# Kernel tuning notes

Hardware: AMD Instinct MI355X
Metric: run time of the kernel (lower is better)

## Reference

```python
import jax, jax.numpy as jnp
import numpy as np

B, C, H, W = 16, 512, 32, 32
NH, HD = 8, 64
CTX_DIM, L = 768, 512
EPS = 1e-5


def setup_inputs() -> dict:
    key = jax.random.key(0)
    ks = jax.random.split(key, 10)
    x = jax.random.normal(ks[0], (B, C, H, W), dtype=jnp.float32)
    context = jax.random.normal(ks[1], (B, L, CTX_DIM), dtype=jnp.float32)
    context_mask = jax.random.randint(ks[2], (B, L), 0, 2).astype(bool)
    context_mask = context_mask.at[:, 0].set(True)  # guarantee >=1 valid key per row
    s = 0.02
    ln_w = jnp.ones((C,), jnp.float32)
    ln_b = jnp.zeros((C,), jnp.float32)
    Wq = jax.random.normal(ks[3], (C, C), jnp.float32) * s
    Wk = jax.random.normal(ks[4], (C, C), jnp.float32) * s
    Wv = jax.random.normal(ks[5], (C, C), jnp.float32) * s
    Wo = jax.random.normal(ks[6], (C, C), jnp.float32) * s
    Wctx = jax.random.normal(ks[7], (C, CTX_DIM), jnp.float32) * s
    return {"x": x, "context": context, "context_mask": context_mask,
            "ln_w": ln_w, "ln_b": ln_b, "Wq": Wq, "Wk": Wk, "Wv": Wv,
            "Wo": Wo, "Wctx": Wctx}


def _layernorm(x, w, b):
    mu = jnp.mean(x, axis=-1, keepdims=True)
    var = jnp.mean(jnp.square(x - mu), axis=-1, keepdims=True)
    return (x - mu) * jax.lax.rsqrt(var + EPS) * w + b


def reference(x, context, context_mask, ln_w, ln_b, Wq, Wk, Wv, Wo, Wctx):
    b, c, h, w = x.shape
    n = h * w
    hidden = x.reshape(b, c, n).transpose(0, 2, 1)          # [b, n, c]
    hidden_norm = _layernorm(hidden, ln_w, ln_b)
    ctx = jnp.einsum('bld,cd->blc', context, Wctx)          # context_proj

    q = jnp.einsum('bnc,ec->bne', hidden_norm, Wq).reshape(b, n, NH, HD).transpose(0, 2, 1, 3)
    k = jnp.einsum('blc,ec->ble', ctx, Wk).reshape(b, -1, NH, HD).transpose(0, 2, 1, 3)
    v = jnp.einsum('blc,ec->ble', ctx, Wv).reshape(b, -1, NH, HD).transpose(0, 2, 1, 3)

    scale = HD ** -0.5
    scores = jnp.einsum('bhnd,bhld->bhnl', q, k) * scale    # [b,H,n,L]
    mask4 = context_mask[:, None, None, :]                  # [b,1,1,L]
    scores = jnp.where(mask4, scores, -jnp.inf)
    all_invalid = ~jnp.any(mask4, axis=-1, keepdims=True)   # [b,1,1,1]
    scores = jnp.where(all_invalid, 0.0, scores)
    attn = jax.nn.softmax(scores, axis=-1)
    attn = jnp.where(mask4, attn, 0.0)
    attn = jnp.where(all_invalid, 0.0, attn)

    out = jnp.einsum('bhnl,bhld->bhnd', attn, v)            # [b,H,n,hd]
    out = out.transpose(0, 2, 1, 3).reshape(b, n, c)
    out = jnp.einsum('bnc,ec->bne', out, Wo)
    out = out + hidden
    return out.transpose(0, 2, 1).reshape(b, c, h, w)
```

## Files before the change

### kernel.cpp

```cpp
#include <hip/hip_runtime.h>

#define B_   16
#define C_   512
#define N_   1024
#define L_   512
#define CTX_ 768
#define NH_  8
#define HD_  64
#define EPS_ 1e-5f

typedef short bfrag  __attribute__((ext_vector_type(8)));
typedef short bfrag4 __attribute__((ext_vector_type(4)));
typedef float f32x4  __attribute__((ext_vector_type(4)));

__device__ __forceinline__ ushort f2bf(float f) {
  union { float f; unsigned u; } v; v.f = f;
  unsigned r = v.u + 0x7fffu + ((v.u >> 16) & 1u);
  return (ushort)(r >> 16);
}

__device__ __forceinline__ f32x4 mfma16(bfrag a, bfrag b, f32x4 c) {
  return __builtin_amdgcn_mfma_f32_16x16x32_bf16(a, b, c, 0, 0, 0);
}
__device__ __forceinline__ f32x4 mfma16k16(bfrag4 a, bfrag4 b, f32x4 c) {
  return __builtin_amdgcn_mfma_f32_16x16x16bf16_1k(a, b, c, 0, 0, 0);
}
__device__ __forceinline__ unsigned cvt_pk_bf16(float lo, float hi) {
  unsigned d;
  asm("v_cvt_pk_bf16_f32 %0, %1, %2" : "=v"(d) : "v"(lo), "v"(hi));
  return d;
}

__device__ __forceinline__ void g2l16(const ushort* g, ushort* l) {
  __builtin_amdgcn_global_load_lds(
      (const __attribute__((address_space(1))) void*)g,
      (__attribute__((address_space(3))) void*)l, 16, 0, 0);
}

__global__ __launch_bounds__(256) void cast6_kernel(
    const float* __restrict__ s0, const float* __restrict__ s1,
    const float* __restrict__ s2, const float* __restrict__ s3,
    const float* __restrict__ s4, const float* __restrict__ s5,
    ushort* __restrict__ d0, ushort* __restrict__ d1, ushort* __restrict__ d2,
    ushort* __restrict__ d3, ushort* __restrict__ d4, ushort* __restrict__ d5) {
  int i = blockIdx.x * 256 + threadIdx.x;
  const float* src; ushort* dst; int off;
  if      (i < 1572864) { src = s0; dst = d0; off = i; }
  else if (i < 1671168) { src = s1; dst = d1; off = i - 1572864; }
  else if (i < 1736704) { src = s2; dst = d2; off = i - 1671168; }
  else if (i < 1802240) { src = s3; dst = d3; off = i - 1736704; }
  else if (i < 1867776) { src = s4; dst = d4; off = i - 1802240; }
  else                  { src = s5; dst = d5; off = i - 1867776; }
  float4 vv = ((const float4*)src)[off];
  ushort4 o;
  o.x = f2bf(vv.x); o.y = f2bf(vv.y); o.z = f2bf(vv.z); o.w = f2bf(vv.w);
  ((ushort4*)dst)[off] = o;
}

__global__ __launch_bounds__(1024) void ln_kernel(const float* __restrict__ x,
                                                  const float* __restrict__ w,
                                                  const float* __restrict__ bia,
                                                  ushort* __restrict__ hn) {
  const int b  = blockIdx.x;
  const int n0 = blockIdx.y * 64;
  const int tid = threadIdx.x;
  const int nx = tid & 63, cg = tid >> 6;
  const float* xb = x + (size_t)b * C_ * N_;

  float s = 0.f, s2 = 0.f;
  for (int c = cg; c < C_; c += 16) {
    float v = xb[(size_t)c * N_ + n0 + nx];
    s += v; s2 += v * v;
  }
  __shared__ float red[2][16][64];
  __shared__ float mean[64], rstd[64];
  red[0][cg][nx] = s; red[1][cg][nx] = s2;
  __syncthreads();
  if (cg == 0) {
    float ss = 0.f, ss2 = 0.f;
#pragma unroll
    for (int i = 0; i < 16; ++i) { ss += red[0][i][nx]; ss2 += red[1][i][nx]; }
    float mu  = ss * (1.f / C_);
    float var = ss2 * (1.f / C_) - mu * mu;
    mean[nx] = mu;
    rstd[nx] = rsqrtf(var + EPS_);
  }
  __syncthreads();

  __shared__ float tile[64][65];
  for (int ct = 0; ct < 8; ++ct) {
    const int c0 = ct * 64;
    for (int cy = cg; cy < 64; cy += 16)
      tile[cy][nx] = xb[(size_t)(c0 + cy) * N_ + n0 + nx];
    __syncthreads();
    const int cx = tid & 63, ng = tid >> 6;
    const float wv = w[c0 + cx], bv = bia[c0 + cx];
    for (int ny = ng; ny < 64; ny += 16) {
      float val = (tile[cx][ny] - mean[ny]) * rstd[ny] * wv + bv;
      hn[((size_t)b * N_ + n0 + ny) * C_ + c0 + cx] = f2bf(val);
    }
    __syncthreads();
  }
}

__device__ __forceinline__ void gemm_core(const ushort* __restrict__ A,
                                          const ushort* __restrict__ W,
                                          int K, ushort* la, ushort* lb,
                                          f32x4 acc[4][4],
                                          int tid, int wm, int we, int col, int rg) {
  const int lane = tid & 63, w = tid >> 6;
  const int rloc = lane >> 2, pt = lane & 3;
  const int pts = pt ^ ((rloc >> 1) & 3);
  const int qsel = (rg ^ ((col >> 1) & 3)) * 8;

  for (int k0 = 0; k0 < K; k0 += 32) {
#pragma unroll
    for (int c = 0; c < 2; ++c) {
      const int chunk = w + c * 4;
      const int row = chunk * 16 + rloc;
      g2l16(A + (size_t)row * K + k0 + pts * 8, la + chunk * 512);
      g2l16(W + (size_t)row * K + k0 + pts * 8, lb + chunk * 512);
    }
    __syncthreads();
    bfrag af[4], bf[4];
#pragma unroll
    for (int i = 0; i < 4; ++i) {
      af[i] = *(const bfrag*)&la[(wm + i * 16 + col) * 32 + qsel];
      bf[i] = *(const bfrag*)&lb[(we + i * 16 + col) * 32 + qsel];
    }
#pragma unroll
    for (int i = 0; i < 4; ++i)
#pragma unroll
      for (int j = 0; j < 4; ++j)
        acc[i][j] = mfma16(af[i], bf[j], acc[i][j]);
    __syncthreads();
  }
}

__global__ __launch_bounds__(256) void gemm_ctxq(const ushort* __restrict__ ctxb,
                                                 const ushort* __restrict__ Wctxb,
                                                 ushort* __restrict__ ctxo,
                                                 const ushort* __restrict__ hn,
                                                 const ushort* __restrict__ Wqb,
                                                 ushort* __restrict__ qo) {
  __shared__ ushort la[128 * 32];
  __shared__ ushort lb[128 * 32];
  const int bid = blockIdx.x;
  const int tid = threadIdx.x, lane = tid & 63, w = tid >> 6;
  const int wm = (w >> 1) * 64, we = (w & 1) * 64;
  const int col = lane & 15, rg = lane >> 4;

  const ushort* A; const ushort* W; ushort* out; int K, m0, e0;
  if (bid < 256) {
    m0 = (bid & 63) * 128; e0 = (bid >> 6) * 128;
    A = ctxb; W = Wctxb; out = ctxo; K = CTX_;
  } else {
    const int b2 = bid - 256;
    m0 = (b2 & 127) * 128; e0 = (b2 >> 7) * 128;
    A = hn; W = Wqb; out = qo; K = C_;
  }

  f32x4 acc[4][4] = {};
  gemm_core(A + (size_t)m0 * K, W + (size_t)e0 * K, K, la, lb, acc, tid, wm, we, col, rg);

#pragma unroll
  for (int i = 0; i < 4; ++i)
#pragma unroll
    for (int j = 0; j < 4; ++j)
#pragma unroll
      for (int r = 0; r < 4; ++r)
        out[(size_t)(m0 + wm + i * 16 + rg * 4 + r) * 512 + e0 + we + j * 16 + col] =
            f2bf(acc[i][j][r]);
}

__global__ __launch_bounds__(256) void gemm_kv(const ushort* __restrict__ A,
                                               const ushort* __restrict__ Wk,
                                               const ushort* __restrict__ Wv,
                                               ushort* __restrict__ Ko,
                                               ushort* __restrict__ Vt_g) {
  __shared__ ushort la[128 * 32];
  __shared__ ushort lb[128 * 32];
  __shared__ float T[16][132];
  const int isv = blockIdx.y >> 2;
  const ushort* W = isv ? Wv : Wk;
  const int m0 = blockIdx.x * 128, e0 = (blockIdx.y & 3) * 128;
  const int tid = threadIdx.x, lane = tid & 63, w = tid >> 6;
  const int wm = (w >> 1) * 64, we = (w & 1) * 64;
  const int col = lane & 15, rg = lane >> 4;

  f32x4 acc[4][4] = {};
  gemm_core(A + (size_t)m0 * C_, W + (size_t)e0 * C_, C_, la, lb, acc, tid, wm, we, col, rg);

  if (!isv) {
#pragma unroll
    for (int i = 0; i < 4; ++i)
#pragma unroll
      for (int j = 0; j < 4; ++j)
#pragma unroll
        for (int r = 0; r < 4; ++r)
          Ko[(size_t)(m0 + wm + i * 16 + rg * 4 + r) * 512 + e0 + we + j * 16 + col] =
              f2bf(acc[i][j][r]);
  } else {
    const int b = m0 >> 9, l0 = m0 & 511;
#pragma unroll
    for (int g = 0; g < 8; ++g) {
      if ((w & 1) == (g >> 2)) {
        const int j = g & 3;
#pragma unroll
        for (int i = 0; i < 4; ++i)
          *(f32x4*)&T[col][wm + i * 16 + rg * 4] = acc[i][j];
      }
      __syncthreads();
      const int n = tid & 127;
      for (int cc = tid >> 7; cc < 16; cc += 2) {
        const int e = e0 + g * 16 + cc;
        Vt_g[((size_t)b * 512 + e) * 512 + l0 + n] = f2bf(T[cc][n]);
      }
      __syncthreads();
    }
  }
}

__global__ __launch_bounds__(256) void gemm_res(const ushort* __restrict__ A,
                                                const ushort* __restrict__ W,
                                                const float* __restrict__ x,
                                                float* __restrict__ out) {
  __shared__ ushort la[128 * 32];
  __shared__ ushort lb[128 * 32];
  __shared__ float T[16][132];
  const int m0 = blockIdx.x * 128, e0 = blockIdx.y * 128;
  const int tid = threadIdx.x, lane = tid & 63, w = tid >> 6;
  const int wm = (w >> 1) * 64, we = (w & 1) * 64;
  const int col = lane & 15, rg = lane >> 4;

  f32x4 acc[4][4] = {};
  gemm_core(A + (size_t)m0 * C_, W + (size_t)e0 * C_, C_, la, lb, acc, tid, wm, we, col, rg);

  const int b = m0 >> 10, n0l = m0 & 1023;
#pragma unroll
  for (int g = 0; g < 8; ++g) {
    if ((w & 1) == (g >> 2)) {
      const int j = g & 3;
#pragma unroll
      for (int i = 0; i < 4; ++i)
        *(f32x4*)&T[col][wm + i * 16 + rg * 4] = acc[i][j];
    }
    __syncthreads();
    const int n = tid & 127;
    for (int cc = tid >> 7; cc < 16; cc += 2) {
      const int c = e0 + g * 16 + cc;
      const size_t idx = (size_t)b * C_ * N_ + (size_t)c * N_ + n0l + n;
      out[idx] = T[cc][n] + x[idx];
    }
    __syncthreads();
  }
}

__global__ __launch_bounds__(256) void attn_mfma(const ushort* __restrict__ q,
                                                 const ushort* __restrict__ k,
                                                 const ushort* __restrict__ vt,
                                                 const int* __restrict__ mask,
                                                 ushort* __restrict__ o) {
  __shared__ ushort Kl[2][64 * 72];
  __shared__ ushort Vt[2][64 * 72];
  __shared__ float mlb[2][64];

  const int lin = blockIdx.x;
  const int hb = lin & 127, qb = lin >> 7;
  const int h = hb & 7, b = hb >> 3;
  const int q0 = qb * 128;
  const int tid = threadIdx.x, lane = tid & 63, w = tid >> 6;
  const int col = lane & 15, rg = lane >> 4;
  const int wq = w * 32;
  const float C1 = 0.18033688011112042f;

  bfrag qf[2][2];
#pragma unroll
  for (int mi = 0; mi < 2; ++mi)
#pragma unroll
    for (int kc = 0; kc < 2; ++kc)
      qf[mi][kc] = *(const bfrag*)
          &q[((size_t)b * N_ + q0 + wq + mi * 16 + col) * C_ + h * HD_ + kc * 32 + rg * 8];

  f32x4 oa[2][4] = {};
  float l_part[2] = {0.f, 0.f};

  {
#pragma unroll
    for (int it = 0; it < 2; ++it) {
      const int idx = it * 256 + tid;
      const int key = idx >> 3, part = idx & 7;
      *(int4*)&Kl[0][key * 72 + part * 8] =
          *(const int4*)&k[((size_t)b * L_ + key) * C_ + h * HD_ + part * 8];
    }
#pragma unroll
    for (int it = 0; it < 2; ++it) {
      const int idx = it * 256 + tid;
      const int d = idx >> 3, k8 = (idx & 7) * 8;
      *(int4*)&Vt[0][d * 72 + k8] =
          *(const int4*)&vt[((size_t)b * 512 + h * HD_ + d) * 512 + k8];
    }
    if (tid < 64) mlb[0][tid] = mask[b * L_ + tid] ? 0.f : -1e30f;
  }
  __syncthreads();

  for (int t = 0; t < 8; ++t) {
    const int cur = t & 1;
    int4 kreg[2];
    int4 vreg[2];
    float mreg = 0.f;
    if (t < 7) {
      const int l0n = (t + 1) * 64;
#pragma unroll
      for (int it = 0; it < 2; ++it) {
        const int idx = it * 256 + tid;
        const int key = idx >> 3, part = idx & 7;
        kreg[it] = *(const int4*)&k[((size_t)b * L_ + l0n + key) * C_ + h * HD_ + part * 8];
      }
#pragma unroll
      for (int it = 0; it < 2; ++it) {
        const int idx = it * 256 + tid;
        const int d = idx >> 3, k8 = (idx & 7) * 8;
        vreg[it] = *(const int4*)&vt[((size_t)b * 512 + h * HD_ + d) * 512 + l0n + k8];
      }
      if (tid < 64) mreg = mask[b * L_ + l0n + tid] ? 0.f : -1e30f;
    }

    const ushort* Kc = &Kl[cur][0];
    const ushort* Vc = &Vt[cur][0];
    f32x4 s2[2][4] = {};
#pragma unroll
    for (int kc = 0; kc < 2; ++kc) {
      bfrag kf[4];
#pragma unroll
      for (int ni = 0; ni < 4; ++ni)
        kf[ni] = *(const bfrag*)&Kc[(ni * 16 + col) * 72 + kc * 32 + rg * 8];
#pragma unroll
      for (int mi = 0; mi < 2; ++mi)
#pragma unroll
        for (int ni = 0; ni < 4; ++ni)
          s2[mi][ni] = mfma16(kf[ni], qf[mi][kc], s2[mi][ni]);
    }
    bfrag4 pf[2][4];
#pragma unroll
    for (int ni = 0; ni < 4; ++ni) {
      const f32x4 bias4 = *(const f32x4*)&mlb[cur][ni * 16 + rg * 4];
#pragma unroll
      for (int mi = 0; mi < 2; ++mi) {
        const float p0 = exp2f(fmaf(s2[mi][ni][0], C1, bias4[0]));
        const float p1 = exp2f(fmaf(s2[mi][ni][1], C1, bias4[1]));
        const float p2 = exp2f(fmaf(s2[mi][ni][2], C1, bias4[2]));
        const float p3 = exp2f(fmaf(s2[mi][ni][3], C1, bias4[3]));
        l_part[mi] += (p0 + p1) + (p2 + p3);
        union { bfrag4 v; unsigned u[2]; } pk;
        pk.u[0] = cvt_pk_bf16(p0, p1);
        pk.u[1] = cvt_pk_bf16(p2, p3);
        pf[mi][ni] = pk.v;
      }
    }
#pragma unroll
    for (int ni = 0; ni < 4; ++ni) {
      bfrag4 vf[4];
#pragma unroll
      for (int di = 0; di < 4; ++di)
        vf[di] = *(const bfrag4*)&Vc[(di * 16 + col) * 72 + ni * 16 + rg * 4];
#pragma unroll
      for (int mi = 0; mi < 2; ++mi)
#pragma unroll
        for (int di = 0; di < 4; ++di)
          oa[mi][di] = mfma16k16(pf[mi][ni], vf[di], oa[mi][di]);
    }

    if (t < 7) {
      const int nb = cur ^ 1;
#pragma unroll
      for (int it = 0; it < 2; ++it) {
        const int idx = it * 256 + tid;
        const int key = idx >> 3, part = idx & 7;
        *(int4*)&Kl[nb][key * 72 + part * 8] = kreg[it];
      }
#pragma unroll
      for (int it = 0; it < 2; ++it) {
        const int idx = it * 256 + tid;
        const int d = idx >> 3, k8 = (idx & 7) * 8;
        *(int4*)&Vt[nb][d * 72 + k8] = vreg[it];
      }
      if (tid < 64) mlb[nb][tid] = mreg;
    }
    __syncthreads();
  }

  float linv[2][4];
#pragma unroll
  for (int mi = 0; mi < 2; ++mi) {
    float l = l_part[mi];
    l += __shfl_xor(l, 16);
    l += __shfl_xor(l, 32);
#pragma unroll
    for (int r = 0; r < 4; ++r) {
      int lv = __builtin_amdgcn_ds_bpermute((rg * 4 + r) * 4, __float_as_int(l));
      linv[mi][r] = 1.f / __int_as_float(lv);
    }
  }
#pragma unroll
  for (int mi = 0; mi < 2; ++mi)
#pragma unroll
    for (int r = 0; r < 4; ++r) {
      const size_t row = (size_t)b * N_ + q0 + wq + mi * 16 + rg * 4 + r;
#pragma unroll
      for (int di = 0; di < 4; ++di)
        o[row * C_ + h * HD_ + di * 16 + col] = f2bf(oa[mi][di][r] * linv[mi][r]);
    }
}

extern "C" void kernel_launch(void* const* d_in, const int* in_sizes, int n_in,
                              void* d_out, int out_size, void* d_ws, size_t ws_size,
                              hipStream_t stream) {
  (void)in_sizes; (void)n_in; (void)out_size; (void)ws_size;
  const float* x       = (const float*)d_in[0];
  const float* context = (const float*)d_in[1];
  const int*   mask    = (const int*)d_in[2];
  const float* ln_w    = (const float*)d_in[3];
  const float* ln_b    = (const float*)d_in[4];
  const float* Wq      = (const float*)d_in[5];
  const float* Wk      = (const float*)d_in[6];
  const float* Wv      = (const float*)d_in[7];
  const float* Wo      = (const float*)d_in[8];
  const float* Wctx    = (const float*)d_in[9];

  char* wsb = (char*)d_ws;
  ushort* qb    = (ushort*)(wsb + 0);
  ushort* kb    = (ushort*)(wsb + 16777216);
  ushort* vb    = (ushort*)(wsb + 25165824);
  ushort* atto  = (ushort*)(wsb + 33554432);
  ushort* ctx   = (ushort*)(wsb + 50331648);
  ushort* wctxb = (ushort*)(wsb + 58720256);
  ushort* wqb   = (ushort*)(wsb + 59506688);
  ushort* wkb   = (ushort*)(wsb + 60030976);
  ushort* wvb   = (ushort*)(wsb + 60555264);
  ushort* wob   = (ushort*)(wsb + 61079552);
  ushort* hn    = (ushort*)(wsb + 61603840);
  ushort* ctxb  = (ushort*)(wsb + 78381056);

  cast6_kernel<<<7552, 256, 0, stream>>>(context, Wctx, Wq, Wk, Wv, Wo,
                                         ctxb, wctxb, wqb, wkb, wvb, wob);
  ln_kernel<<<dim3(B_, N_ / 64), 1024, 0, stream>>>(x, ln_w, ln_b, hn);
  gemm_ctxq<<<768, 256, 0, stream>>>(ctxb, wctxb, ctx, hn, wqb, qb);
  gemm_kv<<<dim3(64, 8), 256, 0, stream>>>(ctx, wkb, wvb, kb, vb);
  attn_mfma<<<1024, 256, 0, stream>>>(qb, kb, vb, mask, atto);
  gemm_res<<<dim3(128, 4), 256, 0, stream>>>(atto, wob, x, (float*)d_out);
}
```

Before: 146.6 us.

## Process two query tiles per attention block to reuse staged K/V

Each attention workgroup now covers 256 query rows instead of 128, so every wave handles two 32-row query sub-tiles against each K/V tile held in shared memory. The grid is halved to 512 blocks. This halves global K/V loads and LDS staging per query row and amortizes barriers across more MFMA work. In exchange it doubles the accumulator and Q-fragment registers per thread, which may lower occupancy, and fewer blocks on 256 CUs gives a coarser load balance.

```diff
diff --git a/kernel.cpp b/kernel.cpp
--- a/kernel.cpp
+++ b/kernel.cpp
@@ -268,22 +268,25 @@
   const int lin = blockIdx.x;
   const int hb = lin & 127, qb = lin >> 7;
   const int h = hb & 7, b = hb >> 3;
-  const int q0 = qb * 128;
+  const int q0 = qb * 256;
   const int tid = threadIdx.x, lane = tid & 63, w = tid >> 6;
   const int col = lane & 15, rg = lane >> 4;
   const int wq = w * 32;
   const float C1 = 0.18033688011112042f;
 
-  bfrag qf[2][2];
-#pragma unroll
-  for (int mi = 0; mi < 2; ++mi)
-#pragma unroll
-    for (int kc = 0; kc < 2; ++kc)
-      qf[mi][kc] = *(const bfrag*)
-          &q[((size_t)b * N_ + q0 + wq + mi * 16 + col) * C_ + h * HD_ + kc * 32 + rg * 8];
-
-  f32x4 oa[2][4] = {};
-  float l_part[2] = {0.f, 0.f};
+  bfrag qf[2][2][2];
+#pragma unroll
+  for (int qs = 0; qs < 2; ++qs)
+#pragma unroll
+    for (int mi = 0; mi < 2; ++mi)
+#pragma unroll
+      for (int kc = 0; kc < 2; ++kc)
+        qf[qs][mi][kc] = *(const bfrag*)
+            &q[((size_t)b * N_ + q0 + qs * 128 + wq + mi * 16 + col) * C_ +
+               h * HD_ + kc * 32 + rg * 8];
+
+  f32x4 oa[2][2][4] = {};
+  float l_part[2][2] = {};
 
   {
 #pragma unroll
@@ -328,47 +331,50 @@
 
     const ushort* Kc = &Kl[cur][0];
     const ushort* Vc = &Vt[cur][0];
-    f32x4 s2[2][4] = {};
-#pragma unroll
-    for (int kc = 0; kc < 2; ++kc) {
-      bfrag kf[4];
-#pragma unroll
-      for (int ni = 0; ni < 4; ++ni)
-        kf[ni] = *(const bfrag*)&Kc[(ni * 16 + col) * 72 + kc * 32 + rg * 8];
-#pragma unroll
-      for (int mi = 0; mi < 2; ++mi)
+#pragma unroll
+    for (int qs = 0; qs < 2; ++qs) {
+      f32x4 s2[2][4] = {};
+#pragma unroll
+      for (int kc = 0; kc < 2; ++kc) {
+        bfrag kf[4];
 #pragma unroll
         for (int ni = 0; ni < 4; ++ni)
-          s2[mi][ni] = mfma16(kf[ni], qf[mi][kc], s2[mi][ni]);
-    }
-    bfrag4 pf[2][4];
-#pragma unroll
-    for (int ni = 0; ni < 4; ++ni) {
-      const f32x4 bias4 = *(const f32x4*)&mlb[cur][ni * 16 + rg * 4];
-#pragma unroll
-      for (int mi = 0; mi < 2; ++mi) {
-        const float p0 = exp2f(fmaf(s2[mi][ni][0], C1, bias4[0]));
-        const float p1 = exp2f(fmaf(s2[mi][ni][1], C1, bias4[1]));
-        const float p2 = exp2f(fmaf(s2[mi][ni][2], C1, bias4[2]));
-        const float p3 = exp2f(fmaf(s2[mi][ni][3], C1, bias4[3]));
-        l_part[mi] += (p0 + p1) + (p2 + p3);
-        union { bfrag4 v; unsigned u[2]; } pk;
-        pk.u[0] = cvt_pk_bf16(p0, p1);
-        pk.u[1] = cvt_pk_bf16(p2, p3);
-        pf[mi][ni] = pk.v;
-      }
-    }
-#pragma unroll
-    for (int ni = 0; ni < 4; ++ni) {
-      bfrag4 vf[4];
-#pragma unroll
-      for (int di = 0; di < 4; ++di)
-        vf[di] = *(const bfrag4*)&Vc[(di * 16 + col) * 72 + ni * 16 + rg * 4];
-#pragma unroll
-      for (int mi = 0; mi < 2; ++mi)
+          kf[ni] = *(const bfrag*)&Kc[(ni * 16 + col) * 72 + kc * 32 + rg * 8];
+#pragma unroll
+        for (int mi = 0; mi < 2; ++mi)
+#pragma unroll
+          for (int ni = 0; ni < 4; ++ni)
+            s2[mi][ni] = mfma16(kf[ni], qf[qs][mi][kc], s2[mi][ni]);
+      }
+      bfrag4 pf[2][4];
+#pragma unroll
+      for (int ni = 0; ni < 4; ++ni) {
+        const f32x4 bias4 = *(const f32x4*)&mlb[cur][ni * 16 + rg * 4];
+#pragma unroll
+        for (int mi = 0; mi < 2; ++mi) {
+          const float p0 = exp2f(fmaf(s2[mi][ni][0], C1, bias4[0]));
+          const float p1 = exp2f(fmaf(s2[mi][ni][1], C1, bias4[1]));
+          const float p2 = exp2f(fmaf(s2[mi][ni][2], C1, bias4[2]));
+          const float p3 = exp2f(fmaf(s2[mi][ni][3], C1, bias4[3]));
+          l_part[qs][mi] += (p0 + p1) + (p2 + p3);
+          union { bfrag4 v; unsigned u[2]; } pk;
+          pk.u[0] = cvt_pk_bf16(p0, p1);
+          pk.u[1] = cvt_pk_bf16(p2, p3);
+          pf[mi][ni] = pk.v;
+        }
+      }
+#pragma unroll
+      for (int ni = 0; ni < 4; ++ni) {
+        bfrag4 vf[4];
 #pragma unroll
         for (int di = 0; di < 4; ++di)
-          oa[mi][di] = mfma16k16(pf[mi][ni], vf[di], oa[mi][di]);
+          vf[di] = *(const bfrag4*)&Vc[(di * 16 + col) * 72 + ni * 16 + rg * 4];
+#pragma unroll
+        for (int mi = 0; mi < 2; ++mi)
+#pragma unroll
+          for (int di = 0; di < 4; ++di)
+            oa[qs][mi][di] = mfma16k16(pf[mi][ni], vf[di], oa[qs][mi][di]);
+      }
     }
 
     if (t < 7) {
@@ -390,27 +396,28 @@
     __syncthreads();
   }
 
-  float linv[2][4];
-#pragma unroll
-  for (int mi = 0; mi < 2; ++mi) {
-    float l = l_part[mi];
-    l += __shfl_xor(l, 16);
-    l += __shfl_xor(l, 32);
-#pragma unroll
-    for (int r = 0; r < 4; ++r) {
-      int lv = __builtin_amdgcn_ds_bpermute((rg * 4 + r) * 4, __float_as_int(l));
-      linv[mi][r] = 1.f / __int_as_float(lv);
-    }
-  }
-#pragma unroll
-  for (int mi = 0; mi < 2; ++mi)
-#pragma unroll
-    for (int r = 0; r < 4; ++r) {
-      const size_t row = (size_t)b * N_ + q0 + wq + mi * 16 + rg * 4 + r;
-#pragma unroll
-      for (int di = 0; di < 4; ++di)
-        o[row * C_ + h * HD_ + di * 16 + col] = f2bf(oa[mi][di][r] * linv[mi][r]);
-    }
+#pragma unroll
+  for (int qs = 0; qs < 2; ++qs) {
+#pragma unroll
+    for (int mi = 0; mi < 2; ++mi) {
+      float l = l_part[qs][mi];
+      l += __shfl_xor(l, 16);
+      l += __shfl_xor(l, 32);
+      float linv[4];
+#pragma unroll
+      for (int r = 0; r < 4; ++r) {
+        int lv = __builtin_amdgcn_ds_bpermute((rg * 4 + r) * 4, __float_as_int(l));
+        linv[r] = 1.f / __int_as_float(lv);
+      }
+#pragma unroll
+      for (int r = 0; r < 4; ++r) {
+        const size_t row = (size_t)b * N_ + q0 + qs * 128 + wq + mi * 16 + rg * 4 + r;
+#pragma unroll
+        for (int di = 0; di < 4; ++di)
+          o[row * C_ + h * HD_ + di * 16 + col] = f2bf(oa[qs][mi][di][r] * linv[r]);
+      }
+    }
+  }
 }
 
 extern "C" void kernel_launch(void* const* d_in, const int* in_sizes, int n_in,
@@ -447,6 +454,6 @@
   ln_kernel<<<dim3(B_, N_ / 64), 1024, 0, stream>>>(x, ln_w, ln_b, hn);
   gemm_ctxq<<<768, 256, 0, stream>>>(ctxb, wctxb, ctx, hn, wqb, qb);
   gemm_kv<<<dim3(64, 8), 256, 0, stream>>>(ctx, wkb, wvb, kb, vb);
-  attn_mfma<<<1024, 256, 0, stream>>>(qb, kb, vb, mask, atto);
+  attn_mfma<<<512, 256, 0, stream>>>(qb, kb, vb, mask, atto);
   gemm_res<<<dim3(128, 4), 256, 0, stream>>>(atto, wob, x, (float*)d_out);
 }
```

Result: slower. 161.9 us (+10.5%).
